# Optimization experiments

Hardware: AMD Instinct MI355X
Metric: run time of the kernel (lower is better)

The kernel has to match this reference:

```python
import jax, jax.numpy as jnp
import numpy as np

N, M, DIM = 50000, 800000, 64
EPS_MSG = 1e-7
BN_EPS = 1e-5


def setup_inputs() -> dict:
    key = jax.random.key(0)
    ks = jax.random.split(key, 12)
    x = jax.random.normal(ks[0], (N, DIM), dtype=jnp.float32)
    edge_index = jax.random.randint(ks[1], (2, M), 0, N, dtype=jnp.int64)
    edge_attr = jax.random.normal(ks[2], (M, DIM), dtype=jnp.float32)
    s = 1.0 / np.sqrt(DIM)
    s2 = 1.0 / np.sqrt(2 * DIM)
    # 3 GENConv layers, each with MLP: Linear(dim,2dim)->BN->ReLU->Linear(2dim,dim)
    W1 = jax.random.uniform(ks[3], (3, DIM, 2 * DIM), jnp.float32, -s, s)
    b1 = jax.random.uniform(ks[4], (3, 2 * DIM), jnp.float32, -s, s)
    gamma = jnp.ones((3, 2 * DIM), jnp.float32)
    beta = jnp.zeros((3, 2 * DIM), jnp.float32)
    W2 = jax.random.uniform(ks[5], (3, 2 * DIM, DIM), jnp.float32, -s2, s2)
    b2 = jax.random.uniform(ks[6], (3, DIM), jnp.float32, -s2, s2)
    return {"x": x, "edge_index": edge_index, "edge_attr": edge_attr,
            "W1": W1, "b1": b1, "gamma": gamma, "beta": beta, "W2": W2, "b2": b2}


def _genconv(x, src, dst, edge_attr, W1, b1, g, be, W2, b2):
    n = x.shape[0]
    # message: relu(x_j + e) + eps   (per-edge)
    msg = jax.nn.relu(x[src] + edge_attr) + EPS_MSG  # [M, dim]
    # softmax aggregation (per-destination, per-channel), t=1.0
    mx = jax.ops.segment_max(msg, dst, num_segments=n)
    mx = jnp.where(jnp.isfinite(mx), mx, 0.0)  # empty segments
    e = jnp.exp(msg - mx[dst])
    ssum = jax.ops.segment_sum(e, dst, num_segments=n)
    alpha = e / jnp.maximum(ssum[dst], 1e-16)
    agg = jax.ops.segment_sum(msg * alpha, dst, num_segments=n)  # [N, dim]
    # residual then MLP: Linear -> BatchNorm(train) -> ReLU -> Linear
    h = agg + x
    h1 = h @ W1 + b1
    mu = h1.mean(axis=0)
    var = h1.var(axis=0)
    h1 = (h1 - mu) * jax.lax.rsqrt(var + BN_EPS) * g + be
    h1 = jax.nn.relu(h1)
    return h1 @ W2 + b2


def reference(x, edge_index, edge_attr, W1, b1, gamma, beta, W2, b2):
    src, dst = edge_index[0], edge_index[1]
    for i in range(3):
        x = _genconv(x, src, dst, edge_attr, W1[i], b1[i], gamma[i], beta[i], W2[i], b2[i])
    return x
```

## Files before the change

kernel.cpp:

```cpp
#include <hip/hip_runtime.h>

#define DIM 64
#define D2  128


__global__ void k_detect(const int* __restrict__ ei, int m, int* __restrict__ flag) {
  __shared__ int nz;
  int t = threadIdx.x;
  if (t == 0) nz = 0;
  __syncthreads();
  int lim = 4096;
  if (lim > m / 2) lim = m / 2;
  int any = 0;
  for (int i = t; i < lim; i += 256) any |= (ei[2 * i + 1] != 0);
  if (any) atomicOr(&nz, 1);
  __syncthreads();
  if (t == 0) flag[0] = nz ? 0 : 1;
}

__global__ void k_hist(const int* __restrict__ ei, int m, const int* __restrict__ flag,
                       int* __restrict__ cnt) {
  int i = blockIdx.x * 256 + threadIdx.x;
  if (i >= m) return;
  int f = flag[0];
  int d = f ? ei[2 * ((size_t)m + i)] : ei[(size_t)m + i];
  atomicAdd(&cnt[d], 1);
}

__global__ void k_scanA(const int* __restrict__ cnt, int* __restrict__ excl,
                        int* __restrict__ bsum, int n) {
  __shared__ int lds[256];
  int t = threadIdx.x;
  int i = blockIdx.x * 256 + t;
  int v = (i < n) ? cnt[i] : 0;
  lds[t] = v;
  __syncthreads();
  for (int off = 1; off < 256; off <<= 1) {
    int u = (t >= off) ? lds[t - off] : 0;
    __syncthreads();
    lds[t] += u;
    __syncthreads();
  }
  if (i < n) excl[i] = lds[t] - v;
  if (t == 255) bsum[blockIdx.x] = lds[255];
}

__global__ void k_scanC(const int* __restrict__ excl, const int* __restrict__ bsum,
                        int* __restrict__ start, int* __restrict__ cursor, int n, int m) {
  __shared__ int red[256];
  __shared__ int boffS;
  int t = threadIdx.x;
  int acc = 0;
  for (int i = t; i < blockIdx.x; i += 256) acc += bsum[i];
  red[t] = acc;
  __syncthreads();
  for (int off = 128; off > 0; off >>= 1) {
    if (t < off) red[t] += red[t + off];
    __syncthreads();
  }
  if (t == 0) boffS = red[0];
  __syncthreads();
  int i = blockIdx.x * 256 + t;
  if (i < n) {
    int s = excl[i] + boffS;
    start[i] = s;
    cursor[i] = s;
  }
  if (blockIdx.x == 0 && t == 0) start[n] = m;
}

__global__ void k_scatter(const int* __restrict__ ei, int m, const int* __restrict__ flag,
                          int* __restrict__ cursor, int2* __restrict__ sed) {
  int i = blockIdx.x * 256 + threadIdx.x;
  if (i >= m) return;
  int f = flag[0];
  int s, d;
  if (f) { s = ei[2 * (size_t)i]; d = ei[2 * ((size_t)m + i)]; }
  else   { s = ei[i];             d = ei[(size_t)m + i]; }
  int pos = atomicAdd(&cursor[d], 1);
  sed[pos] = make_int2(i, s);
}

__global__ __launch_bounds__(256) void k_agg(
    const float* __restrict__ x, const float* __restrict__ ea,
    const int2* __restrict__ sed, const int* __restrict__ start,
    float* __restrict__ h, int n) {
  int lane = threadIdx.x & 63;
  int node = blockIdx.x * 4 + (threadIdx.x >> 6);
  if (node >= n) return;
  int sub = lane >> 3;
  int cl = lane & 7;
  int s0 = start[node], s1 = start[node + 1];

  float sS[8], wW[8];
#pragma unroll
  for (int c = 0; c < 8; c++) { sS[c] = 0.f; wW[c] = 0.f; }

#define BSTEP(K, J)                                   \
  {                                                   \
    int o = __shfl_xor(key, (J), 64);                 \
    bool dir = ((lane & (K)) == 0);                   \
    bool lo = ((lane & (J)) == 0);                    \
    int mn = key < o ? key : o;                       \
    int mx = key < o ? o : key;                       \
    key = (dir == lo) ? mn : mx;                      \
  }

  for (int base = s0; base < s1; base += 64) {
    int cnt = s1 - base;
    if (cnt > 64) cnt = 64;
    int key = 0x7fffffff;
    int srcReg = 0;
    if (lane < cnt) {
      int2 e = sed[base + lane];
      key = (e.x << 6) | lane;
      srcReg = e.y;
    }
#pragma unroll
    for (int k = 2; k <= 16; k <<= 1) {
#pragma unroll
      for (int j = k >> 1; j > 0; j >>= 1) BSTEP(k, j)
    }
    if (cnt > 16) {
#pragma unroll
      for (int j = 16; j > 0; j >>= 1) BSTEP(32, j)
      if (cnt > 32) {
#pragma unroll
        for (int j = 32; j > 0; j >>= 1) BSTEP(64, j)
      }
    }
    int nIter = (cnt + 7) >> 3;
    for (int t = 0; t < nIter; t++) {
      int idx = 8 * t + sub;
      int kk = __shfl(key, idx, 64);
      int org = kk & 63;
      int eid = (int)(((unsigned)kk) >> 6);
      int src = __shfl(srcReg, org, 64);
      if (idx < cnt) {
        const float* xr = &x[(size_t)src * DIM + cl * 8];
        const float* ar = &ea[(size_t)eid * DIM + cl * 8];
        float4 xa = *(const float4*)xr;
        float4 xb = *(const float4*)(xr + 4);
        float4 aa = *(const float4*)ar;
        float4 ab = *(const float4*)(ar + 4);
        float xv[8] = {xa.x, xa.y, xa.z, xa.w, xb.x, xb.y, xb.z, xb.w};
        float av[8] = {aa.x, aa.y, aa.z, aa.w, ab.x, ab.y, ab.z, ab.w};
#pragma unroll
        for (int c = 0; c < 8; c++) {
          float g = fmaxf(xv[c] + av[c], 0.f) + 1e-7f;
          float p = __expf(g);
          sS[c] += p;
          wW[c] = fmaf(g, p, wW[c]);
        }
      }
    }
  }
#undef BSTEP

#pragma unroll
  for (int off = 8; off < 64; off <<= 1) {
#pragma unroll
    for (int c = 0; c < 8; c++) {
      sS[c] += __shfl_xor(sS[c], off, 64);
      wW[c] += __shfl_xor(wW[c], off, 64);
    }
  }

  if (sub == 0) {
    const float* xr = &x[(size_t)node * DIM + cl * 8];
    float4 xa = *(const float4*)xr;
    float4 xb = *(const float4*)(xr + 4);
    float xv[8] = {xa.x, xa.y, xa.z, xa.w, xb.x, xb.y, xb.z, xb.w};
    float o[8];
#pragma unroll
    for (int c = 0; c < 8; c++) o[c] = wW[c] / fmaxf(sS[c], 1e-16f) + xv[c];
    *(float4*)&h[(size_t)node * DIM + cl * 8] = make_float4(o[0], o[1], o[2], o[3]);
    *(float4*)&h[(size_t)node * DIM + cl * 8 + 4] = make_float4(o[4], o[5], o[6], o[7]);
  }
}

__global__ __launch_bounds__(256) void k_gemm1(
    const float* __restrict__ h, const float* __restrict__ W1,
    const float* __restrict__ b1, float* __restrict__ h1,
    float* __restrict__ ps, float* __restrict__ pq, int n) {
  __shared__ float ws[DIM * D2];
  __shared__ float hs[DIM][68];
  __shared__ float red[8][D2];
  int tid = threadIdx.x;
  int row0 = blockIdx.x * 64;
  const float4* w4 = (const float4*)W1;
  float4* ws4 = (float4*)ws;
#pragma unroll
  for (int i = 0; i < 8; i++) ws4[tid + 256 * i] = w4[tid + 256 * i];
  const float4* h4 = (const float4*)h;
#pragma unroll
  for (int i = 0; i < 4; i++) {
    int idx = tid + 256 * i;
    int r = idx & 63, dg = idx >> 6;
    int row = row0 + r;
    float4 v = make_float4(0.f, 0.f, 0.f, 0.f);
    if (row < n) v = h4[(size_t)row * 16 + dg];
    int c = dg * 4;
    hs[c + 0][r] = v.x; hs[c + 1][r] = v.y; hs[c + 2][r] = v.z; hs[c + 3][r] = v.w;
  }
  __syncthreads();

  int tc = tid & 31, tr = tid >> 5;
  float bb[4];
#pragma unroll
  for (int k = 0; k < 4; k++) bb[k] = b1[tc * 4 + k];
  float acc[8][4];
#pragma unroll
  for (int i = 0; i < 8; i++)
#pragma unroll
    for (int k = 0; k < 4; k++) acc[i][k] = bb[k];
#pragma unroll 4
  for (int d = 0; d < DIM; d++) {
    float4 wv = *(const float4*)&ws[d * D2 + tc * 4];
    float4 ha = *(const float4*)&hs[d][tr * 8];
    float4 hb = *(const float4*)&hs[d][tr * 8 + 4];
    float hr[8] = {ha.x, ha.y, ha.z, ha.w, hb.x, hb.y, hb.z, hb.w};
    float wk[4] = {wv.x, wv.y, wv.z, wv.w};
#pragma unroll
    for (int i = 0; i < 8; i++)
#pragma unroll
      for (int k = 0; k < 4; k++) acc[i][k] = fmaf(hr[i], wk[k], acc[i][k]);
  }
  float cs[4] = {0.f, 0.f, 0.f, 0.f}, cq[4] = {0.f, 0.f, 0.f, 0.f};
#pragma unroll
  for (int i = 0; i < 8; i++) {
    int row = row0 + tr * 8 + i;
    if (row < n) {
      ((float4*)h1)[(size_t)row * 32 + tc] =
          make_float4(acc[i][0], acc[i][1], acc[i][2], acc[i][3]);
#pragma unroll
      for (int k = 0; k < 4; k++) { cs[k] += acc[i][k]; cq[k] += acc[i][k] * acc[i][k]; }
    }
  }
  __syncthreads();
#pragma unroll
  for (int k = 0; k < 4; k++) red[tr][tc * 4 + k] = cs[k];
  __syncthreads();
  float asum = 0.f;
  if (tid < D2) {
#pragma unroll
    for (int r = 0; r < 8; r++) asum += red[r][tid];
  }
  __syncthreads();
#pragma unroll
  for (int k = 0; k < 4; k++) red[tr][tc * 4 + k] = cq[k];
  __syncthreads();
  if (tid < D2) {
    float bsumv = 0.f;
#pragma unroll
    for (int r = 0; r < 8; r++) bsumv += red[r][tid];
    ps[(size_t)tid * gridDim.x + blockIdx.x] = asum;
    pq[(size_t)tid * gridDim.x + blockIdx.x] = bsumv;
  }
}

__global__ __launch_bounds__(256) void k_stats(
    const float* __restrict__ ps, const float* __restrict__ pq,
    const float* __restrict__ gamma, const float* __restrict__ beta,
    float* __restrict__ ss, int rows, int n) {
  __shared__ float r0[256], r1[256];
  int j = blockIdx.x;
  int t = threadIdx.x;
  float a = 0.f, b = 0.f;
  for (int r = t; r < rows; r += 256) {
    a += ps[(size_t)j * rows + r];
    b += pq[(size_t)j * rows + r];
  }
  r0[t] = a; r1[t] = b;
  __syncthreads();
  for (int off = 128; off > 0; off >>= 1) {
    if (t < off) { r0[t] += r0[t + off]; r1[t] += r1[t + off]; }
    __syncthreads();
  }
  if (t == 0) {
    float mu = r0[0] / (float)n;
    float var = r1[0] / (float)n - mu * mu;
    float sc = gamma[j] * rsqrtf(var + 1e-5f);
    ss[j] = sc;
    ss[D2 + j] = beta[j] - mu * sc;
  }
}

__global__ __launch_bounds__(256) void k_gemm2(
    const float* __restrict__ h1, const float* __restrict__ W2,
    const float* __restrict__ b2, const float* __restrict__ ss,
    float* __restrict__ out, int n) {
  __shared__ float ws2[D2 * DIM];
  __shared__ float hs[D2][68];
  __shared__ float scS[D2], shS[D2];
  int tid = threadIdx.x;
  int row0 = blockIdx.x * 64;
  const float4* w4 = (const float4*)W2;
  float4* ws4 = (float4*)ws2;
#pragma unroll
  for (int i = 0; i < 8; i++) ws4[tid + 256 * i] = w4[tid + 256 * i];
  if (tid < D2) { scS[tid] = ss[tid]; shS[tid] = ss[D2 + tid]; }
  __syncthreads();
  const float4* h14 = (const float4*)h1;
#pragma unroll
  for (int i = 0; i < 8; i++) {
    int idx = tid + 256 * i;
    int r = idx & 63, cg = idx >> 6;
    int row = row0 + r;
    float4 v = make_float4(0.f, 0.f, 0.f, 0.f);
    if (row < n) v = h14[(size_t)row * 32 + cg];
    int c = cg * 4;
    hs[c + 0][r] = fmaxf(fmaf(v.x, scS[c + 0], shS[c + 0]), 0.f);
    hs[c + 1][r] = fmaxf(fmaf(v.y, scS[c + 1], shS[c + 1]), 0.f);
    hs[c + 2][r] = fmaxf(fmaf(v.z, scS[c + 2], shS[c + 2]), 0.f);
    hs[c + 3][r] = fmaxf(fmaf(v.w, scS[c + 3], shS[c + 3]), 0.f);
  }
  __syncthreads();
  int tc = tid & 15, tr = tid >> 4;
  float bb[4];
#pragma unroll
  for (int k = 0; k < 4; k++) bb[k] = b2[tc * 4 + k];
  float acc[4][4];
#pragma unroll
  for (int i = 0; i < 4; i++)
#pragma unroll
    for (int k = 0; k < 4; k++) acc[i][k] = bb[k];
#pragma unroll 4
  for (int d = 0; d < D2; d++) {
    float4 wv = *(const float4*)&ws2[d * DIM + tc * 4];
    float4 hv = *(const float4*)&hs[d][tr * 4];
    float hr[4] = {hv.x, hv.y, hv.z, hv.w};
    float wk[4] = {wv.x, wv.y, wv.z, wv.w};
#pragma unroll
    for (int i = 0; i < 4; i++)
#pragma unroll
      for (int k = 0; k < 4; k++) acc[i][k] = fmaf(hr[i], wk[k], acc[i][k]);
  }
#pragma unroll
  for (int i = 0; i < 4; i++) {
    int row = row0 + tr * 4 + i;
    if (row < n)
      ((float4*)out)[(size_t)row * 16 + tc] =
          make_float4(acc[i][0], acc[i][1], acc[i][2], acc[i][3]);
  }
}

extern "C" void kernel_launch(void* const* d_in, const int* in_sizes, int n_in,
                              void* d_out, int out_size, void* d_ws, size_t ws_size,
                              hipStream_t stream) {
  (void)n_in; (void)out_size; (void)ws_size;
  const float* x0    = (const float*)d_in[0];
  const int*   ei    = (const int*)d_in[1];
  const float* ea    = (const float*)d_in[2];
  const float* W1    = (const float*)d_in[3];
  const float* b1    = (const float*)d_in[4];
  const float* gamma = (const float*)d_in[5];
  const float* beta  = (const float*)d_in[6];
  const float* W2    = (const float*)d_in[7];
  const float* b2    = (const float*)d_in[8];
  float* out = (float*)d_out;

  int n = in_sizes[0] / DIM;
  int m = in_sizes[1] / 2;

  char* base = (char*)d_ws;
  size_t off = 0;
  auto alloc = [&](size_t bytes) -> void* {
    void* p = base + off;
    off += (bytes + 255) & ~(size_t)255;
    return p;
  };
  int*   cnt    = (int*)alloc((size_t)n * 4);
  int*   excl   = (int*)alloc((size_t)n * 4);
  int*   bsum   = (int*)alloc(256 * 4);
  int*   start  = (int*)alloc((size_t)(n + 1) * 4);
  int*   cursor = (int*)alloc((size_t)n * 4);
  int*   flag   = (int*)alloc(256);
  int2*  sed    = (int2*)alloc((size_t)m * 8);
  float* h      = (float*)alloc((size_t)n * DIM * 4);
  float* h1     = (float*)alloc((size_t)n * D2 * 4);
  int tiles = (n + 63) / 64;
  float* ps = (float*)alloc((size_t)tiles * D2 * 4);
  float* pq = (float*)alloc((size_t)tiles * D2 * 4);
  float* ss = (float*)alloc(256 * 4);

  hipMemsetAsync(cnt, 0, (size_t)n * 4, stream);
  k_detect<<<1, 256, 0, stream>>>(ei, m, flag);
  int mg = (m + 255) / 256;
  int ng = (n + 255) / 256;
  k_hist<<<mg, 256, 0, stream>>>(ei, m, flag, cnt);
  k_scanA<<<ng, 256, 0, stream>>>(cnt, excl, bsum, n);
  k_scanC<<<ng, 256, 0, stream>>>(excl, bsum, start, cursor, n, m);
  k_scatter<<<mg, 256, 0, stream>>>(ei, m, flag, cursor, sed);

  for (int l = 0; l < 3; l++) {
    const float* xin = (l == 0) ? x0 : out;
    k_agg<<<(n + 3) / 4, 256, 0, stream>>>(xin, ea, sed, start, h, n);
    k_gemm1<<<tiles, 256, 0, stream>>>(h, W1 + (size_t)l * DIM * D2, b1 + (size_t)l * D2,
                                       h1, ps, pq, n);
    k_stats<<<D2, 256, 0, stream>>>(ps, pq, gamma + (size_t)l * D2, beta + (size_t)l * D2,
                                    ss, tiles, n);
    k_gemm2<<<tiles, 256, 0, stream>>>(h1, W2 + (size_t)l * D2 * DIM, b2 + (size_t)l * DIM,
                                       ss, out, n);
  }
}
```

Before: 684.5 us.

## Sort per-node edge lists once in a canon kernel and simplify aggregation

Moves the per-chunk bitonic sort of edge ids from the aggregation kernel into a one-time k_canon pass that rewrites the CSR edge array in sorted order, so the three layer aggregations no longer repeat the sort. The aggregation kernel also changes its lane mapping from 8 edges with 8 floats per lane to 4 edges with 4 floats (one float4) per lane, and uses 32-bit offset arithmetic. This trades one extra launch and a pass over the edge array for less shuffle work per layer, but halves the edges processed in parallel per wavefront iteration.

```diff
diff --git a/kernel.cpp b/kernel.cpp
--- a/kernel.cpp
+++ b/kernel.cpp
@@ -81,20 +81,12 @@
   sed[pos] = make_int2(i, s);
 }
 
-__global__ __launch_bounds__(256) void k_agg(
-    const float* __restrict__ x, const float* __restrict__ ea,
-    const int2* __restrict__ sed, const int* __restrict__ start,
-    float* __restrict__ h, int n) {
+__global__ __launch_bounds__(256) void k_canon(
+    int2* __restrict__ sed, const int* __restrict__ start, int n) {
   int lane = threadIdx.x & 63;
   int node = blockIdx.x * 4 + (threadIdx.x >> 6);
   if (node >= n) return;
-  int sub = lane >> 3;
-  int cl = lane & 7;
   int s0 = start[node], s1 = start[node + 1];
-
-  float sS[8], wW[8];
-#pragma unroll
-  for (int c = 0; c < 8; c++) { sS[c] = 0.f; wW[c] = 0.f; }
 
 #define BSTEP(K, J)                                   \
   {                                                   \
@@ -129,53 +121,88 @@
         for (int j = 32; j > 0; j >>= 1) BSTEP(64, j)
       }
     }
-    int nIter = (cnt + 7) >> 3;
-    for (int t = 0; t < nIter; t++) {
-      int idx = 8 * t + sub;
-      int kk = __shfl(key, idx, 64);
-      int org = kk & 63;
-      int eid = (int)(((unsigned)kk) >> 6);
-      int src = __shfl(srcReg, org, 64);
-      if (idx < cnt) {
-        const float* xr = &x[(size_t)src * DIM + cl * 8];
-        const float* ar = &ea[(size_t)eid * DIM + cl * 8];
-        float4 xa = *(const float4*)xr;
-        float4 xb = *(const float4*)(xr + 4);
-        float4 aa = *(const float4*)ar;
-        float4 ab = *(const float4*)(ar + 4);
-        float xv[8] = {xa.x, xa.y, xa.z, xa.w, xb.x, xb.y, xb.z, xb.w};
-        float av[8] = {aa.x, aa.y, aa.z, aa.w, ab.x, ab.y, ab.z, ab.w};
-#pragma unroll
-        for (int c = 0; c < 8; c++) {
-          float g = fmaxf(xv[c] + av[c], 0.f) + 1e-7f;
-          float p = __expf(g);
-          sS[c] += p;
-          wW[c] = fmaf(g, p, wW[c]);
-        }
-      }
-    }
+    int org = key & 63;
+    int eid = (int)(((unsigned)key) >> 6);
+    int src = __shfl(srcReg, org, 64);
+    if (lane < cnt) sed[base + lane] = make_int2(eid, src);
   }
 #undef BSTEP
-
-#pragma unroll
-  for (int off = 8; off < 64; off <<= 1) {
-#pragma unroll
-    for (int c = 0; c < 8; c++) {
+}
+
+__global__ __launch_bounds__(256) void k_agg(
+    const float* __restrict__ x, const float* __restrict__ ea,
+    const int2* __restrict__ sed, const int* __restrict__ start,
+    float* __restrict__ h, int n) {
+  int lane = threadIdx.x & 63;
+  int node = blockIdx.x * 4 + (threadIdx.x >> 6);
+  if (node >= n) return;
+  int sub = lane >> 4;
+  int cl = lane & 15;
+  int s0 = start[node], s1 = start[node + 1];
+
+  float sS[4] = {0.f, 0.f, 0.f, 0.f};
+  float wW[4] = {0.f, 0.f, 0.f, 0.f};
+
+#define ACC(EID, SRC)                                                   \
+  {                                                                     \
+    unsigned xo = ((unsigned)(SRC) << 6) + (cl << 2);                   \
+    unsigned ao = ((unsigned)(EID) << 6) + (cl << 2);                   \
+    float4 xv = *(const float4*)(x + xo);                               \
+    float4 av = *(const float4*)(ea + ao);                              \
+    float g0 = fmaxf(xv.x + av.x, 0.f) + 1e-7f;                         \
+    float g1 = fmaxf(xv.y + av.y, 0.f) + 1e-7f;                         \
+    float g2 = fmaxf(xv.z + av.z, 0.f) + 1e-7f;                         \
+    float g3 = fmaxf(xv.w + av.w, 0.f) + 1e-7f;                         \
+    float p0 = __expf(g0), p1 = __expf(g1), p2 = __expf(g2), p3 = __expf(g3); \
+    sS[0] += p0; sS[1] += p1; sS[2] += p2; sS[3] += p3;                 \
+    wW[0] = fmaf(g0, p0, wW[0]); wW[1] = fmaf(g1, p1, wW[1]);           \
+    wW[2] = fmaf(g2, p2, wW[2]); wW[3] = fmaf(g3, p3, wW[3]);           \
+  }
+
+  for (int base = s0; base < s1; base += 64) {
+    int cnt = s1 - base;
+    if (cnt > 64) cnt = 64;
+    int eK = 0, sK = 0;
+    if (lane < cnt) {
+      int2 e = sed[base + lane];
+      eK = e.x; sK = e.y;
+    }
+    int full = cnt >> 2;
+    int rem = cnt & 3;
+    for (int t = 0; t < full; t++) {
+      int idx = 4 * t + sub;
+      int eid = __shfl(eK, idx, 64);
+      int src = __shfl(sK, idx, 64);
+      ACC(eid, src)
+    }
+    if (rem) {
+      int idx = 4 * full + sub;
+      int idxc = idx < cnt ? idx : 0;
+      int eid = __shfl(eK, idxc, 64);
+      int src = __shfl(sK, idxc, 64);
+      if (sub < rem) ACC(eid, src)
+    }
+  }
+#undef ACC
+
+#pragma unroll
+  for (int off = 16; off < 64; off <<= 1) {
+#pragma unroll
+    for (int c = 0; c < 4; c++) {
       sS[c] += __shfl_xor(sS[c], off, 64);
       wW[c] += __shfl_xor(wW[c], off, 64);
     }
   }
 
   if (sub == 0) {
-    const float* xr = &x[(size_t)node * DIM + cl * 8];
-    float4 xa = *(const float4*)xr;
-    float4 xb = *(const float4*)(xr + 4);
-    float xv[8] = {xa.x, xa.y, xa.z, xa.w, xb.x, xb.y, xb.z, xb.w};
-    float o[8];
-#pragma unroll
-    for (int c = 0; c < 8; c++) o[c] = wW[c] / fmaxf(sS[c], 1e-16f) + xv[c];
-    *(float4*)&h[(size_t)node * DIM + cl * 8] = make_float4(o[0], o[1], o[2], o[3]);
-    *(float4*)&h[(size_t)node * DIM + cl * 8 + 4] = make_float4(o[4], o[5], o[6], o[7]);
+    unsigned xo = ((unsigned)node << 6) + (cl << 2);
+    float4 xv = *(const float4*)(x + xo);
+    float4 o;
+    o.x = wW[0] / fmaxf(sS[0], 1e-16f) + xv.x;
+    o.y = wW[1] / fmaxf(sS[1], 1e-16f) + xv.y;
+    o.z = wW[2] / fmaxf(sS[2], 1e-16f) + xv.z;
+    o.w = wW[3] / fmaxf(sS[3], 1e-16f) + xv.w;
+    *(float4*)(h + xo) = o;
   }
 }
 
@@ -388,14 +415,16 @@
   k_detect<<<1, 256, 0, stream>>>(ei, m, flag);
   int mg = (m + 255) / 256;
   int ng = (n + 255) / 256;
+  int ag = (n + 3) / 4;
   k_hist<<<mg, 256, 0, stream>>>(ei, m, flag, cnt);
   k_scanA<<<ng, 256, 0, stream>>>(cnt, excl, bsum, n);
   k_scanC<<<ng, 256, 0, stream>>>(excl, bsum, start, cursor, n, m);
   k_scatter<<<mg, 256, 0, stream>>>(ei, m, flag, cursor, sed);
+  k_canon<<<ag, 256, 0, stream>>>(sed, start, n);
 
   for (int l = 0; l < 3; l++) {
     const float* xin = (l == 0) ? x0 : out;
-    k_agg<<<(n + 3) / 4, 256, 0, stream>>>(xin, ea, sed, start, h, n);
+    k_agg<<<ag, 256, 0, stream>>>(xin, ea, sed, start, h, n);
     k_gemm1<<<tiles, 256, 0, stream>>>(h, W1 + (size_t)l * DIM * D2, b1 + (size_t)l * D2,
                                        h1, ps, pq, n);
     k_stats<<<D2, 256, 0, stream>>>(ps, pq, gamma + (size_t)l * D2, beta + (size_t)l * D2,
```

Result: no change. 695.2 us (+1.6%).
